# Kernel optimization log

Measured on AMD Instinct MI355X. Metric: run time of the kernel, lower is better.

Reference implementation:

```python
import math
import jax, jax.numpy as jnp
import numpy as np

DIM = 192
HEADS = 8
C_RATIO = 0.5
CR = int(DIM * C_RATIO)          # 96
HD = DIM // HEADS                # 24
CRH = CR // HEADS                # 12
SCALE = (HD * C_RATIO) ** -0.5   # qk_scale default


def conv2d(x, w, b, stride, pad, groups):
    # x: [B,C,H,W], w: [O, C//groups, kh, kw]
    y = jax.lax.conv_general_dilated(
        x, w, (stride, stride), [(pad, pad), (pad, pad)],
        dimension_numbers=('NCHW', 'OIHW', 'NCHW'),
        feature_group_count=groups)
    return y + b[None, :, None, None]


def layernorm(x, g, b, eps=1e-5):
    mu = jnp.mean(x, axis=-1, keepdims=True)
    var = jnp.mean((x - mu) ** 2, axis=-1, keepdims=True)
    return (x - mu) * jax.lax.rsqrt(var + eps) * g + b


def setup_inputs() -> dict:
    key = jax.random.key(0)
    ks = jax.random.split(key, 10)
    B, H, W = 16, 128, 128
    N = H * W
    p = lambda k, shape: jax.random.normal(k, shape, jnp.float32) * 0.02
    return {
        'x': jax.random.normal(ks[0], (B, N, DIM), jnp.float32),
        'H': H, 'W': W,
        'red_w': p(ks[1], (DIM, 1, 4, 4)), 'red_b': jnp.zeros((DIM,), jnp.float32),
        'dw_w': p(ks[2], (DIM, 1, 3, 3)), 'dw_b': jnp.zeros((DIM,), jnp.float32),
        'conv_w': p(ks[3], (DIM, DIM, 1, 1)), 'conv_b': jnp.zeros((DIM,), jnp.float32),
        'ln_g': jnp.ones((DIM,), jnp.float32), 'ln_b': jnp.zeros((DIM,), jnp.float32),
        'q_w': p(ks[4], (DIM, DIM)),
        'k_w': p(ks[5], (CR, DIM)),
        'v_w': p(ks[6], (CR, DIM)),
        'cpe_w': p(ks[7], (CR, 1, 3, 3)), 'cpe_b': jnp.zeros((CR,), jnp.float32),
        'proj_w': p(ks[8], (DIM, DIM)), 'proj_b': jnp.zeros((DIM,), jnp.float32),
    }


def reference(x, H, W, red_w, red_b, dw_w, dw_b, conv_w, conv_b,
              ln_g, ln_b, q_w, k_w, v_w, cpe_w, cpe_b, proj_w, proj_b):
    B, N, C = x.shape
    # eval-mode recursion depth (self.training == False branch)
    _time = max(int(math.log(H // 16, 4)), int(math.log(W // 16, 4)))
    _time = max(_time, 2)

    _x = jnp.swapaxes(x, 1, 2).reshape(B, C, H, W)
    for _ in range(_time):                        # recursive stride-4 depthwise reduction
        _x = conv2d(_x, red_w, red_b, 4, 0, C)
    _x = conv2d(_x, dw_w, dw_b, 1, 1, C)          # depthwise 3x3
    _x = conv2d(_x, conv_w, conv_b, 1, 0, 1)      # 1x1 mix
    _x = jnp.swapaxes(_x.reshape(B, C, -1), 1, 2)  # [B, M, C]
    _x = jax.nn.gelu(layernorm(_x, ln_g, ln_b), approximate=False)
    M = _x.shape[1]

    q = (_x @ q_w.T).reshape(B, M, HEADS, HD).transpose(0, 2, 1, 3)    # [B,h,M,hd]
    k = (_x @ k_w.T).reshape(B, M, HEADS, CRH).transpose(0, 2, 1, 3)   # [B,h,M,crh]
    v = (x @ v_w.T).reshape(B, N, HEADS, CRH).transpose(0, 2, 1, 3)    # [B,h,N,crh]

    # channel-axis attention: q^T k over reduced tokens M -> [B,h,hd,crh]
    attn = jax.nn.softmax(jnp.einsum('bhmd,bhme->bhde', q, k) * SCALE, axis=-1)

    # CPE: depthwise conv over v arranged as [B, CR, H, W], added back to v
    v_img = jnp.swapaxes(v, 1, 2).reshape(B, N, CR).transpose(0, 2, 1).reshape(B, CR, H, W)
    cpe = conv2d(v_img, cpe_w, cpe_b, 1, 1, CR).reshape(B, HEADS, CRH, N)
    v = v + jnp.swapaxes(cpe, -1, -2)             # [B,h,N,crh]

    out = jnp.einsum('bhde,bhne->bhdn', attn, v)  # attn @ v^T -> [B,h,hd,N]
    # replicate torch: .transpose(1,2).reshape(B,N,-1)
    out = jnp.swapaxes(out, 1, 2).reshape(B, N, C)
    return out @ proj_w.T + proj_b
```

## Files before the change

### kernel.cpp

```cpp
#include <hip/hip_runtime.h>
#include <hip/hip_bf16.h>
#include <math.h>

#define NB 16
#define HIMG 128
#define WIMG 128
#define NTOK 16384
#define CDIM 192
#define CRDIM 96
#define NHEAD 8
#define HDIM 24
#define CRHD 12
#define MRED 64
#define SCALE_QK 0.28867513459481287f

typedef __bf16 bf16x8 __attribute__((ext_vector_type(8)));
typedef __bf16 bf16x4 __attribute__((ext_vector_type(4)));
typedef float f32x4 __attribute__((ext_vector_type(4)));

__global__ void k_prep(const float* __restrict__ vw, const float* __restrict__ pw,
                       __bf16* __restrict__ wb) {
    int i = blockIdx.x * 256 + threadIdx.x;
    if (i < CRDIM * CDIM) wb[i] = (__bf16)vw[i];
    else if (i < CRDIM * CDIM + CDIM * CDIM) wb[i] = (__bf16)pw[i - CRDIM * CDIM];
}

__global__ __launch_bounds__(256) void k_reduce(const float* __restrict__ x,
                                                const float* __restrict__ rw,
                                                const float* __restrict__ rb,
                                                float* __restrict__ y1) {
    int idx = blockIdx.x * 256 + threadIdx.x;
    int c4 = idx % 48;
    int t  = idx / 48;
    int m  = t & 63;
    int b  = t >> 6;
    float w[16][4];
#pragma unroll
    for (int e = 0; e < 4; ++e)
#pragma unroll
        for (int i = 0; i < 16; ++i) w[i][e] = rw[(c4 * 4 + e) * 16 + i];
    int py = m >> 3, px = m & 7;
    const float4* xb = (const float4*)(x + (long)b * NTOK * CDIM) + c4;
    float acc[4] = {0.f, 0.f, 0.f, 0.f};
    for (int a = 0; a < 16; ++a) {
        const float4* xrow = xb + (long)((py * 16 + a) * WIMG + px * 16) * 48;
#pragma unroll
        for (int bb = 0; bb < 16; ++bb) {
            float4 vv = xrow[(long)bb * 48];
            int i1 = ((a >> 2) << 2) + (bb >> 2);
            int i2 = ((a & 3) << 2) + (bb & 3);
            acc[0] += w[i1][0] * w[i2][0] * vv.x;
            acc[1] += w[i1][1] * w[i2][1] * vv.y;
            acc[2] += w[i1][2] * w[i2][2] * vv.z;
            acc[3] += w[i1][3] * w[i2][3] * vv.w;
        }
    }
    float4 outv;
#pragma unroll
    for (int e = 0; e < 4; ++e) {
        float S = 0.f;
#pragma unroll
        for (int i = 0; i < 16; ++i) S += w[i][e];
        acc[e] += rb[c4 * 4 + e] * (S + 1.f);
        ((float*)&outv)[e] = acc[e];
    }
    ((float4*)(y1 + (long)(b * MRED + m) * CDIM))[c4] = outv;
}

__global__ void k_dwmix(const float* __restrict__ y1, const float* __restrict__ dww,
                        const float* __restrict__ dwb, const float* __restrict__ cw,
                        const float* __restrict__ cb, const float* __restrict__ lg,
                        const float* __restrict__ lb, float* __restrict__ xr) {
    __shared__ float sT[CDIM];
    __shared__ float sU[CDIM];
    int m = blockIdx.x, b = blockIdx.y, c = threadIdx.x;
    int py = m >> 3, px = m & 7;
    float t = dwb[c];
#pragma unroll
    for (int ki = 0; ki < 3; ++ki)
#pragma unroll
        for (int kj = 0; kj < 3; ++kj) {
            int yy = py + ki - 1, xx = px + kj - 1;
            if (yy >= 0 && yy < 8 && xx >= 0 && xx < 8)
                t += dww[c * 9 + ki * 3 + kj] * y1[(b * MRED + yy * 8 + xx) * CDIM + c];
        }
    sT[c] = t;
    __syncthreads();
    float u = cb[c];
    for (int cc = 0; cc < CDIM; ++cc) u += cw[c * CDIM + cc] * sT[cc];
    sU[c] = u;
    __syncthreads();
    float s = 0.f, s2 = 0.f;
    for (int cc = 0; cc < CDIM; ++cc) { float vv = sU[cc]; s += vv; s2 += vv * vv; }
    float mu = s * (1.f / CDIM);
    float var = fmaxf(s2 * (1.f / CDIM) - mu * mu, 0.f);
    float xh = (u - mu) * rsqrtf(var + 1e-5f);
    float g = xh * lg[c] + lb[c];
    float ge = 0.5f * g * (1.f + erff(g * 0.70710678118654752440f));
    xr[(b * MRED + m) * CDIM + c] = ge;
}

__global__ void k_qk(const float* __restrict__ xr, const float* __restrict__ qw,
                     const float* __restrict__ kw, float* __restrict__ q,
                     float* __restrict__ k) {
    __shared__ float sx[8 * 193];
    int mg = blockIdx.x;
    int b = blockIdx.y;
    int tid = threadIdx.x;
    const float* src = xr + (b * MRED + mg * 8) * CDIM;
    for (int i = tid; i < 8 * CDIM; i += 256) sx[(i / CDIM) * 193 + (i % CDIM)] = src[i];
    __syncthreads();
    for (int oi = tid; oi < 1536 + 768; oi += 256) {
        if (oi < 1536) {
            int d = oi >> 3, mi = oi & 7;
            const float* wr = qw + d * CDIM;
            const float* xs = sx + mi * 193;
            float acc = 0.f;
            for (int c = 0; c < CDIM; ++c) acc += xs[c] * wr[c];
            q[(b * MRED + mg * 8 + mi) * CDIM + d] = acc;
        } else {
            int oj = oi - 1536;
            int e = oj >> 3, mi = oj & 7;
            const float* wr = kw + e * CDIM;
            const float* xs = sx + mi * 193;
            float acc = 0.f;
            for (int c = 0; c < CDIM; ++c) acc += xs[c] * wr[c];
            k[(b * MRED + mg * 8 + mi) * CRDIM + e] = acc;
        }
    }
}

__global__ void k_attn(const float* __restrict__ q, const float* __restrict__ k,
                       float* __restrict__ attn) {
    __shared__ float sL[HDIM * CRHD];
    int h = blockIdx.x, b = blockIdx.y;
    int tid = threadIdx.x;
    for (int i = tid; i < HDIM * CRHD; i += 256) {
        int d = i / CRHD, e = i % CRHD;
        float acc = 0.f;
        for (int m = 0; m < MRED; ++m)
            acc += q[(b * MRED + m) * CDIM + h * HDIM + d] *
                   k[(b * MRED + m) * CRDIM + h * CRHD + e];
        sL[i] = acc * SCALE_QK;
    }
    __syncthreads();
    if (tid < HDIM) {
        float mx = -1e30f;
#pragma unroll
        for (int e = 0; e < CRHD; ++e) mx = fmaxf(mx, sL[tid * CRHD + e]);
        float ex[CRHD]; float sum = 0.f;
#pragma unroll
        for (int e = 0; e < CRHD; ++e) { ex[e] = expf(sL[tid * CRHD + e] - mx); sum += ex[e]; }
        float inv = 1.f / sum;
#pragma unroll
        for (int e = 0; e < CRHD; ++e)
            attn[((b * NHEAD + h) * HDIM + tid) * CRHD + e] = ex[e] * inv;
    }
}

template <int NOUT, bool ABF16, bool OUTBF16, bool BIAS>
__global__ __launch_bounds__(256) void k_gemm(const void* __restrict__ Asrc,
                                              const __bf16* __restrict__ Wb,
                                              const float* __restrict__ bias,
                                              void* __restrict__ Out) {
    static_assert(NOUT % 16 == 0, "");
    constexpr int NF = NOUT / 16;
    __shared__ __bf16 sA[64 * 200];
    __shared__ __bf16 sB[NOUT * 40];
    const int tid = threadIdx.x;
    const long rowbase = (long)blockIdx.x * 64;
    if (ABF16) {
        const __bf16* A = (const __bf16*)Asrc + rowbase * CDIM;
        for (int i = tid; i < 64 * 24; i += 256) {
            int r = i / 24, c8 = i % 24;
            bf16x8 vv = *(const bf16x8*)(A + (long)r * CDIM + c8 * 8);
            *(bf16x8*)(sA + r * 200 + c8 * 8) = vv;
        }
    } else {
        const float* A = (const float*)Asrc + rowbase * CDIM;
        for (int i = tid; i < 64 * 24; i += 256) {
            int r = i / 24, c8 = i % 24;
            const float4* src = (const float4*)(A + (long)r * CDIM + c8 * 8);
            float4 lo = src[0], hi = src[1];
            bf16x8 vv;
            vv[0] = (__bf16)lo.x; vv[1] = (__bf16)lo.y; vv[2] = (__bf16)lo.z; vv[3] = (__bf16)lo.w;
            vv[4] = (__bf16)hi.x; vv[5] = (__bf16)hi.y; vv[6] = (__bf16)hi.z; vv[7] = (__bf16)hi.w;
            *(bf16x8*)(sA + r * 200 + c8 * 8) = vv;
        }
    }
    const int lane = tid & 63, wv = tid >> 6;
    const int l16 = lane & 15, lq = lane >> 4;
    f32x4 acc[NF];
#pragma unroll
    for (int nf = 0; nf < NF; ++nf) acc[nf] = (f32x4){0.f, 0.f, 0.f, 0.f};
    const __bf16* aptr = sA + (wv * 16 + l16) * 200 + lq * 8;
    for (int kc = 0; kc < 6; ++kc) {
        __syncthreads();
        for (int i = tid; i < NOUT * 4; i += 256) {
            int r = i >> 2, c8 = i & 3;
            bf16x8 vv = *(const bf16x8*)(Wb + (long)r * CDIM + kc * 32 + c8 * 8);
            *(bf16x8*)(sB + r * 40 + c8 * 8) = vv;
        }
        __syncthreads();
        bf16x8 af = *(const bf16x8*)(aptr + kc * 32);
#pragma unroll
        for (int nf = 0; nf < NF; ++nf) {
            bf16x8 bfv = *(const bf16x8*)(sB + (nf * 16 + l16) * 40 + lq * 8);
            acc[nf] = __builtin_amdgcn_mfma_f32_16x16x32_bf16(af, bfv, acc[nf], 0, 0, 0);
        }
    }
    const long orow0 = rowbase + wv * 16 + lq * 4;
#pragma unroll
    for (int nf = 0; nf < NF; ++nf) {
        int col = nf * 16 + l16;
        float bv = BIAS ? bias[col] : 0.f;
#pragma unroll
        for (int j = 0; j < 4; ++j) {
            float val = acc[nf][j] + bv;
            long idx = (orow0 + j) * NOUT + col;
            if (OUTBF16) ((__bf16*)Out)[idx] = (__bf16)val;
            else ((float*)Out)[idx] = val;
        }
    }
}

__global__ __launch_bounds__(256) void k_cpe(const __bf16* __restrict__ v,
                                             const float* __restrict__ cw,
                                             const float* __restrict__ cb,
                                             __bf16* __restrict__ vp) {
    int idx = blockIdx.x * 256 + threadIdx.x;
    int g  = idx % 12;
    int t  = idx / 12;
    int x  = t & 127;
    int sb = t >> 7;
    int strip = sb & 15;
    int b  = sb >> 4;
    float w[9][8];
    float bias[8];
#pragma unroll
    for (int e = 0; e < 8; ++e) {
        bias[e] = cb[g * 8 + e];
#pragma unroll
        for (int tp = 0; tp < 9; ++tp) w[tp][e] = cw[(g * 8 + e) * 9 + tp];
    }
    const __bf16* vb = v + (long)b * NTOK * CRDIM + g * 8;
    __bf16* vpb = vp + (long)b * NTOK * CRDIM + g * 8;
    for (int yi = 0; yi < 8; ++yi) {
        int y = strip * 8 + yi;
        bf16x8 cv = *(const bf16x8*)(vb + (long)(y * WIMG + x) * CRDIM);
        float acc[8];
#pragma unroll
        for (int e = 0; e < 8; ++e) acc[e] = (float)cv[e] + bias[e];
#pragma unroll
        for (int ky = 0; ky < 3; ++ky) {
            int yy = y + ky - 1;
            if (yy < 0 || yy >= HIMG) continue;
#pragma unroll
            for (int kx = 0; kx < 3; ++kx) {
                int xx = x + kx - 1;
                if (xx < 0 || xx >= WIMG) continue;
                bf16x8 tv = (ky == 1 && kx == 1) ? cv
                          : *(const bf16x8*)(vb + (long)(yy * WIMG + xx) * CRDIM);
#pragma unroll
                for (int e = 0; e < 8; ++e) acc[e] += w[ky * 3 + kx][e] * (float)tv[e];
            }
        }
        bf16x8 ov;
#pragma unroll
        for (int e = 0; e < 8; ++e) ov[e] = (__bf16)acc[e];
        *(bf16x8*)(vpb + (long)(y * WIMG + x) * CRDIM) = ov;
    }
}

__global__ __launch_bounds__(256) void k_av(const __bf16* __restrict__ vp,
                                            const float* __restrict__ attn,
                                            __bf16* __restrict__ O) {
    __shared__ float sAttn[NHEAD * HDIM * CRHD];
    int chunk = blockIdx.x, b = blockIdx.y;
    int tid = threadIdx.x;
    for (int i = tid; i < NHEAD * HDIM * CRHD; i += 256)
        sAttn[i] = attn[b * NHEAD * HDIM * CRHD + i];
    __syncthreads();
    int n = chunk * 256 + tid;
    const __bf16* vrow = vp + ((long)b * NTOK + n) * CRDIM;
    __bf16* ob = O + (long)b * (HDIM * NHEAD * NTOK);
    for (int h = 0; h < NHEAD; ++h) {
        bf16x4 v0 = *(const bf16x4*)(vrow + h * CRHD);
        bf16x4 v1 = *(const bf16x4*)(vrow + h * CRHD + 4);
        bf16x4 v2 = *(const bf16x4*)(vrow + h * CRHD + 8);
        float pv[CRHD];
#pragma unroll
        for (int e = 0; e < 4; ++e) {
            pv[e] = (float)v0[e]; pv[4 + e] = (float)v1[e]; pv[8 + e] = (float)v2[e];
        }
        const float* ar = sAttn + h * HDIM * CRHD;
#pragma unroll
        for (int d = 0; d < HDIM; ++d) {
            float s = 0.f;
#pragma unroll
            for (int e = 0; e < CRHD; ++e) s += ar[d * CRHD + e] * pv[e];
            ob[(long)(d * NHEAD + h) * NTOK + n] = (__bf16)s;
        }
    }
}

extern "C" void kernel_launch(void* const* d_in, const int* in_sizes, int n_in,
                              void* d_out, int out_size, void* d_ws, size_t ws_size,
                              hipStream_t stream) {
    const float* x      = (const float*)d_in[0];
    const float* red_w  = (const float*)d_in[3];
    const float* red_b  = (const float*)d_in[4];
    const float* dw_w   = (const float*)d_in[5];
    const float* dw_b   = (const float*)d_in[6];
    const float* conv_w = (const float*)d_in[7];
    const float* conv_b = (const float*)d_in[8];
    const float* ln_g   = (const float*)d_in[9];
    const float* ln_b   = (const float*)d_in[10];
    const float* q_w    = (const float*)d_in[11];
    const float* k_w    = (const float*)d_in[12];
    const float* v_w    = (const float*)d_in[13];
    const float* cpe_w  = (const float*)d_in[14];
    const float* cpe_b  = (const float*)d_in[15];
    const float* proj_w = (const float*)d_in[16];
    const float* proj_b = (const float*)d_in[17];
    float* out = (float*)d_out;

    char* ws = (char*)d_ws;
    __bf16* wb_v = (__bf16*)ws;
    __bf16* wb_p = wb_v + CRDIM * CDIM;
    char* R = ws + 110592;
    float*  y1   = (float*)(R + 0);
    float*  xr   = (float*)(R + 786432);
    float*  qb   = (float*)(R + 1572864);
    float*  kb   = (float*)(R + 2359296);
    __bf16* v    = (__bf16*)(R + 2752512);
    __bf16* O    = (__bf16*)(R + 0);
    float*  attn = (float*)(ws + 110592 + 100663296);
    __bf16* vp   = (__bf16*)(ws + 110592 + 100663296 + 147456);

    k_prep<<<216, 256, 0, stream>>>(v_w, proj_w, wb_v);
    k_reduce<<<192, 256, 0, stream>>>(x, red_w, red_b, y1);
    k_dwmix<<<dim3(64, 16), 192, 0, stream>>>(y1, dw_w, dw_b, conv_w, conv_b, ln_g, ln_b, xr);
    k_qk<<<dim3(8, 16), 256, 0, stream>>>(xr, q_w, k_w, qb, kb);
    k_attn<<<dim3(8, 16), 256, 0, stream>>>(qb, kb, attn);
    k_gemm<CRDIM, false, true, false><<<4096, 256, 0, stream>>>(x, wb_v, nullptr, v);
    k_cpe<<<1536, 256, 0, stream>>>(v, cpe_w, cpe_b, vp);
    k_av<<<dim3(64, 16), 256, 0, stream>>>(vp, attn, O);
    k_gemm<CDIM, true, false, true><<<4096, 256, 0, stream>>>(O, wb_p, proj_b, out);
}
```

Baseline: 698.0 us.

## Fuse CPE into AV, merge QK with attention, restructure GEMM and reduction

Several changes land together. The stride-4 reduction now uses 1024 blocks, each splitting its 16 rows across 4 thread groups with a shared-memory sum, so far more parallelism is exposed. Q/K projection and channel attention become one kernel that keeps Q and K in shared memory. The CPE depthwise conv is fused into the attn@v kernel, with each thread handling two adjacent pixels, which removes the vp intermediate and one launch. The GEMM now loads the whole weight slice into LDS once, each wave computes a 2x3 MFMA tile, and the projection GEMM is split across two column halves. Costs are more LDS per block and recomputed v loads per head in the fused kernel.

Result: no change. 693.2 us (-0.7%).

```diff
diff --git a/kernel.cpp b/kernel.cpp
--- a/kernel.cpp
+++ b/kernel.cpp
@@ -16,6 +16,7 @@
 
 typedef __bf16 bf16x8 __attribute__((ext_vector_type(8)));
 typedef __bf16 bf16x4 __attribute__((ext_vector_type(4)));
+typedef __bf16 bf16x2 __attribute__((ext_vector_type(2)));
 typedef float f32x4 __attribute__((ext_vector_type(4)));
 
 __global__ void k_prep(const float* __restrict__ vw, const float* __restrict__ pw,
@@ -25,15 +26,14 @@
     else if (i < CRDIM * CDIM + CDIM * CDIM) wb[i] = (__bf16)pw[i - CRDIM * CDIM];
 }
 
-__global__ __launch_bounds__(256) void k_reduce(const float* __restrict__ x,
+__global__ __launch_bounds__(192) void k_reduce(const float* __restrict__ x,
                                                 const float* __restrict__ rw,
                                                 const float* __restrict__ rb,
                                                 float* __restrict__ y1) {
-    int idx = blockIdx.x * 256 + threadIdx.x;
-    int c4 = idx % 48;
-    int t  = idx / 48;
-    int m  = t & 63;
-    int b  = t >> 6;
+    __shared__ float4 sRed[4][48];
+    int tid = threadIdx.x;
+    int c4 = tid % 48, a4 = tid / 48;
+    int m = blockIdx.x & 63, b = blockIdx.x >> 6;
     float w[16][4];
 #pragma unroll
     for (int e = 0; e < 4; ++e)
@@ -42,7 +42,9 @@
     int py = m >> 3, px = m & 7;
     const float4* xb = (const float4*)(x + (long)b * NTOK * CDIM) + c4;
     float acc[4] = {0.f, 0.f, 0.f, 0.f};
-    for (int a = 0; a < 16; ++a) {
+#pragma unroll
+    for (int ai = 0; ai < 4; ++ai) {
+        int a = a4 * 4 + ai;
         const float4* xrow = xb + (long)((py * 16 + a) * WIMG + px * 16) * 48;
 #pragma unroll
         for (int bb = 0; bb < 16; ++bb) {
@@ -55,16 +57,22 @@
             acc[3] += w[i1][3] * w[i2][3] * vv.w;
         }
     }
-    float4 outv;
-#pragma unroll
-    for (int e = 0; e < 4; ++e) {
-        float S = 0.f;
-#pragma unroll
-        for (int i = 0; i < 16; ++i) S += w[i][e];
-        acc[e] += rb[c4 * 4 + e] * (S + 1.f);
-        ((float*)&outv)[e] = acc[e];
-    }
-    ((float4*)(y1 + (long)(b * MRED + m) * CDIM))[c4] = outv;
+    sRed[a4][c4] = make_float4(acc[0], acc[1], acc[2], acc[3]);
+    __syncthreads();
+    if (a4 == 0) {
+        float4 t0 = sRed[0][c4], t1 = sRed[1][c4], t2 = sRed[2][c4], t3 = sRed[3][c4];
+        float4 outv;
+        float r[4] = {t0.x + t1.x + t2.x + t3.x, t0.y + t1.y + t2.y + t3.y,
+                      t0.z + t1.z + t2.z + t3.z, t0.w + t1.w + t2.w + t3.w};
+#pragma unroll
+        for (int e = 0; e < 4; ++e) {
+            float S = 0.f;
+#pragma unroll
+            for (int i = 0; i < 16; ++i) S += w[i][e];
+            ((float*)&outv)[e] = r[e] + rb[c4 * 4 + e] * (S + 1.f);
+        }
+        ((float4*)(y1 + (long)(b * MRED + m) * CDIM))[c4] = outv;
+    }
 }
 
 __global__ void k_dwmix(const float* __restrict__ y1, const float* __restrict__ dww,
@@ -100,48 +108,32 @@
     xr[(b * MRED + m) * CDIM + c] = ge;
 }
 
-__global__ void k_qk(const float* __restrict__ xr, const float* __restrict__ qw,
-                     const float* __restrict__ kw, float* __restrict__ q,
-                     float* __restrict__ k) {
-    __shared__ float sx[8 * 193];
-    int mg = blockIdx.x;
-    int b = blockIdx.y;
-    int tid = threadIdx.x;
-    const float* src = xr + (b * MRED + mg * 8) * CDIM;
-    for (int i = tid; i < 8 * CDIM; i += 256) sx[(i / CDIM) * 193 + (i % CDIM)] = src[i];
-    __syncthreads();
-    for (int oi = tid; oi < 1536 + 768; oi += 256) {
-        if (oi < 1536) {
-            int d = oi >> 3, mi = oi & 7;
-            const float* wr = qw + d * CDIM;
-            const float* xs = sx + mi * 193;
-            float acc = 0.f;
-            for (int c = 0; c < CDIM; ++c) acc += xs[c] * wr[c];
-            q[(b * MRED + mg * 8 + mi) * CDIM + d] = acc;
-        } else {
-            int oj = oi - 1536;
-            int e = oj >> 3, mi = oj & 7;
-            const float* wr = kw + e * CDIM;
-            const float* xs = sx + mi * 193;
-            float acc = 0.f;
-            for (int c = 0; c < CDIM; ++c) acc += xs[c] * wr[c];
-            k[(b * MRED + mg * 8 + mi) * CRDIM + e] = acc;
-        }
-    }
-}
-
-__global__ void k_attn(const float* __restrict__ q, const float* __restrict__ k,
-                       float* __restrict__ attn) {
+__global__ __launch_bounds__(256) void k_qkattn(const float* __restrict__ xr,
+                                                const float* __restrict__ qw,
+                                                const float* __restrict__ kw,
+                                                float* __restrict__ attn) {
+    __shared__ float sX[64 * 193];
+    __shared__ float sQK[36 * 65];
     __shared__ float sL[HDIM * CRHD];
-    int h = blockIdx.x, b = blockIdx.y;
-    int tid = threadIdx.x;
-    for (int i = tid; i < HDIM * CRHD; i += 256) {
-        int d = i / CRHD, e = i % CRHD;
+    int h = blockIdx.x, b = blockIdx.y, tid = threadIdx.x;
+    const float* src = xr + (long)b * MRED * CDIM;
+    for (int i = tid; i < MRED * CDIM; i += 256) sX[(i / CDIM) * 193 + (i % CDIM)] = src[i];
+    __syncthreads();
+    for (int oi = tid; oi < 36 * 64; oi += 256) {
+        int col = oi >> 6, tok = oi & 63;
+        const float* wr = (col < 24) ? (qw + (long)(h * HDIM + col) * CDIM)
+                                     : (kw + (long)(h * CRHD + (col - 24)) * CDIM);
+        const float* xs = sX + tok * 193;
         float acc = 0.f;
-        for (int m = 0; m < MRED; ++m)
-            acc += q[(b * MRED + m) * CDIM + h * HDIM + d] *
-                   k[(b * MRED + m) * CRDIM + h * CRHD + e];
-        sL[i] = acc * SCALE_QK;
+        for (int c = 0; c < CDIM; ++c) acc += xs[c] * wr[c];
+        sQK[col * 65 + tok] = acc;
+    }
+    __syncthreads();
+    for (int oi = tid; oi < HDIM * CRHD; oi += 256) {
+        int d = oi / CRHD, e = oi % CRHD;
+        float acc = 0.f;
+        for (int t = 0; t < 64; ++t) acc += sQK[d * 65 + t] * sQK[(24 + e) * 65 + t];
+        sL[oi] = acc * SCALE_QK;
     }
     __syncthreads();
     if (tid < HDIM) {
@@ -158,148 +150,162 @@
     }
 }
 
-template <int NOUT, bool ABF16, bool OUTBF16, bool BIAS>
+template <int NOUT, int NSPLIT, bool ABF16, bool OUTBF16, bool BIAS>
 __global__ __launch_bounds__(256) void k_gemm(const void* __restrict__ Asrc,
                                               const __bf16* __restrict__ Wb,
                                               const float* __restrict__ bias,
                                               void* __restrict__ Out) {
-    static_assert(NOUT % 16 == 0, "");
-    constexpr int NF = NOUT / 16;
+    constexpr int NC = NOUT / NSPLIT;
+    constexpr int NFW = 3;
     __shared__ __bf16 sA[64 * 200];
-    __shared__ __bf16 sB[NOUT * 40];
+    __shared__ __bf16 sB[NC * 200];
     const int tid = threadIdx.x;
-    const long rowbase = (long)blockIdx.x * 64;
+    const int nh = (NSPLIT > 1) ? (int)(blockIdx.x % NSPLIT) : 0;
+    const long tile = (NSPLIT > 1) ? (blockIdx.x / NSPLIT) : blockIdx.x;
+    const long rowbase = tile * 64;
     if (ABF16) {
         const __bf16* A = (const __bf16*)Asrc + rowbase * CDIM;
         for (int i = tid; i < 64 * 24; i += 256) {
             int r = i / 24, c8 = i % 24;
-            bf16x8 vv = *(const bf16x8*)(A + (long)r * CDIM + c8 * 8);
-            *(bf16x8*)(sA + r * 200 + c8 * 8) = vv;
+            *(bf16x8*)(sA + r * 200 + c8 * 8) = *(const bf16x8*)(A + (long)r * CDIM + c8 * 8);
         }
     } else {
         const float* A = (const float*)Asrc + rowbase * CDIM;
         for (int i = tid; i < 64 * 24; i += 256) {
             int r = i / 24, c8 = i % 24;
-            const float4* src = (const float4*)(A + (long)r * CDIM + c8 * 8);
-            float4 lo = src[0], hi = src[1];
+            const float4* s4 = (const float4*)(A + (long)r * CDIM + c8 * 8);
+            float4 lo = s4[0], hi = s4[1];
             bf16x8 vv;
             vv[0] = (__bf16)lo.x; vv[1] = (__bf16)lo.y; vv[2] = (__bf16)lo.z; vv[3] = (__bf16)lo.w;
             vv[4] = (__bf16)hi.x; vv[5] = (__bf16)hi.y; vv[6] = (__bf16)hi.z; vv[7] = (__bf16)hi.w;
             *(bf16x8*)(sA + r * 200 + c8 * 8) = vv;
         }
     }
+    for (int i = tid; i < NC * 24; i += 256) {
+        int r = i / 24, c8 = i % 24;
+        *(bf16x8*)(sB + r * 200 + c8 * 8) =
+            *(const bf16x8*)(Wb + (long)(nh * NC + r) * CDIM + c8 * 8);
+    }
+    __syncthreads();
     const int lane = tid & 63, wv = tid >> 6;
     const int l16 = lane & 15, lq = lane >> 4;
-    f32x4 acc[NF];
-#pragma unroll
-    for (int nf = 0; nf < NF; ++nf) acc[nf] = (f32x4){0.f, 0.f, 0.f, 0.f};
-    const __bf16* aptr = sA + (wv * 16 + l16) * 200 + lq * 8;
-    for (int kc = 0; kc < 6; ++kc) {
-        __syncthreads();
-        for (int i = tid; i < NOUT * 4; i += 256) {
-            int r = i >> 2, c8 = i & 3;
-            bf16x8 vv = *(const bf16x8*)(Wb + (long)r * CDIM + kc * 32 + c8 * 8);
-            *(bf16x8*)(sB + r * 40 + c8 * 8) = vv;
-        }
-        __syncthreads();
-        bf16x8 af = *(const bf16x8*)(aptr + kc * 32);
-#pragma unroll
-        for (int nf = 0; nf < NF; ++nf) {
-            bf16x8 bfv = *(const bf16x8*)(sB + (nf * 16 + l16) * 40 + lq * 8);
-            acc[nf] = __builtin_amdgcn_mfma_f32_16x16x32_bf16(af, bfv, acc[nf], 0, 0, 0);
-        }
-    }
-    const long orow0 = rowbase + wv * 16 + lq * 4;
-#pragma unroll
-    for (int nf = 0; nf < NF; ++nf) {
-        int col = nf * 16 + l16;
-        float bv = BIAS ? bias[col] : 0.f;
-#pragma unroll
-        for (int j = 0; j < 4; ++j) {
-            float val = acc[nf][j] + bv;
-            long idx = (orow0 + j) * NOUT + col;
-            if (OUTBF16) ((__bf16*)Out)[idx] = (__bf16)val;
-            else ((float*)Out)[idx] = val;
-        }
-    }
-}
-
-__global__ __launch_bounds__(256) void k_cpe(const __bf16* __restrict__ v,
-                                             const float* __restrict__ cw,
-                                             const float* __restrict__ cb,
-                                             __bf16* __restrict__ vp) {
-    int idx = blockIdx.x * 256 + threadIdx.x;
-    int g  = idx % 12;
-    int t  = idx / 12;
-    int x  = t & 127;
-    int sb = t >> 7;
-    int strip = sb & 15;
-    int b  = sb >> 4;
-    float w[9][8];
-    float bias[8];
-#pragma unroll
-    for (int e = 0; e < 8; ++e) {
-        bias[e] = cb[g * 8 + e];
-#pragma unroll
-        for (int tp = 0; tp < 9; ++tp) w[tp][e] = cw[(g * 8 + e) * 9 + tp];
-    }
-    const __bf16* vb = v + (long)b * NTOK * CRDIM + g * 8;
-    __bf16* vpb = vp + (long)b * NTOK * CRDIM + g * 8;
-    for (int yi = 0; yi < 8; ++yi) {
-        int y = strip * 8 + yi;
-        bf16x8 cv = *(const bf16x8*)(vb + (long)(y * WIMG + x) * CRDIM);
-        float acc[8];
-#pragma unroll
-        for (int e = 0; e < 8; ++e) acc[e] = (float)cv[e] + bias[e];
-#pragma unroll
-        for (int ky = 0; ky < 3; ++ky) {
-            int yy = y + ky - 1;
-            if (yy < 0 || yy >= HIMG) continue;
-#pragma unroll
-            for (int kx = 0; kx < 3; ++kx) {
-                int xx = x + kx - 1;
-                if (xx < 0 || xx >= WIMG) continue;
-                bf16x8 tv = (ky == 1 && kx == 1) ? cv
-                          : *(const bf16x8*)(vb + (long)(yy * WIMG + xx) * CRDIM);
-#pragma unroll
-                for (int e = 0; e < 8; ++e) acc[e] += w[ky * 3 + kx][e] * (float)tv[e];
+    const int mi0 = (wv >> 1) * 2;
+    const int nf0 = (wv & 1) * 3;
+    f32x4 acc[2][NFW];
+#pragma unroll
+    for (int mi = 0; mi < 2; ++mi)
+#pragma unroll
+        for (int nf = 0; nf < NFW; ++nf) acc[mi][nf] = (f32x4){0.f, 0.f, 0.f, 0.f};
+    bf16x8 afr[2][6];
+#pragma unroll
+    for (int mi = 0; mi < 2; ++mi)
+#pragma unroll
+        for (int kc = 0; kc < 6; ++kc)
+            afr[mi][kc] = *(const bf16x8*)(sA + ((mi0 + mi) * 16 + l16) * 200 + kc * 32 + lq * 8);
+#pragma unroll
+    for (int kc = 0; kc < 6; ++kc)
+#pragma unroll
+        for (int nf = 0; nf < NFW; ++nf) {
+            bf16x8 bfv = *(const bf16x8*)(sB + ((nf0 + nf) * 16 + l16) * 200 + kc * 32 + lq * 8);
+#pragma unroll
+            for (int mi = 0; mi < 2; ++mi)
+                acc[mi][nf] = __builtin_amdgcn_mfma_f32_16x16x32_bf16(afr[mi][kc], bfv,
+                                                                      acc[mi][nf], 0, 0, 0);
+        }
+#pragma unroll
+    for (int mi = 0; mi < 2; ++mi) {
+        const long orow0 = rowbase + (mi0 + mi) * 16 + lq * 4;
+#pragma unroll
+        for (int nf = 0; nf < NFW; ++nf) {
+            int col = nh * NC + (nf0 + nf) * 16 + l16;
+            float bv = BIAS ? bias[col] : 0.f;
+#pragma unroll
+            for (int j = 0; j < 4; ++j) {
+                float val = acc[mi][nf][j] + bv;
+                long idx = (orow0 + j) * NOUT + col;
+                if (OUTBF16) ((__bf16*)Out)[idx] = (__bf16)val;
+                else ((float*)Out)[idx] = val;
             }
         }
-        bf16x8 ov;
-#pragma unroll
-        for (int e = 0; e < 8; ++e) ov[e] = (__bf16)acc[e];
-        *(bf16x8*)(vpb + (long)(y * WIMG + x) * CRDIM) = ov;
-    }
-}
-
-__global__ __launch_bounds__(256) void k_av(const __bf16* __restrict__ vp,
-                                            const float* __restrict__ attn,
-                                            __bf16* __restrict__ O) {
-    __shared__ float sAttn[NHEAD * HDIM * CRHD];
-    int chunk = blockIdx.x, b = blockIdx.y;
-    int tid = threadIdx.x;
+    }
+}
+
+__global__ __launch_bounds__(256) void k_avcpe(const __bf16* __restrict__ v,
+                                               const float* __restrict__ attn,
+                                               const float* __restrict__ cw,
+                                               const float* __restrict__ cb,
+                                               __bf16* __restrict__ O) {
+    __shared__ float sA2[NHEAD * HDIM * CRHD];
+    __shared__ float sW[CRDIM * 9];
+    __shared__ float sB2[CRDIM];
+    int chunk = blockIdx.x, b = blockIdx.y, tid = threadIdx.x;
     for (int i = tid; i < NHEAD * HDIM * CRHD; i += 256)
-        sAttn[i] = attn[b * NHEAD * HDIM * CRHD + i];
-    __syncthreads();
-    int n = chunk * 256 + tid;
-    const __bf16* vrow = vp + ((long)b * NTOK + n) * CRDIM;
-    __bf16* ob = O + (long)b * (HDIM * NHEAD * NTOK);
+        sA2[i] = attn[b * NHEAD * HDIM * CRHD + i];
+    for (int i = tid; i < CRDIM * 9; i += 256) sW[i] = cw[i];
+    if (tid < CRDIM) sB2[tid] = cb[tid];
+    __syncthreads();
+    int n0 = (chunk * 256 + tid) * 2;
+    int y = n0 >> 7, x = n0 & 127;
+    bool xm = (x > 0), xp = (x + 2 < WIMG);
+    const __bf16* vb = v + (long)b * NTOK * CRDIM;
+    __bf16* ob = O + (long)b * (CDIM * NTOK);
+#pragma unroll
     for (int h = 0; h < NHEAD; ++h) {
-        bf16x4 v0 = *(const bf16x4*)(vrow + h * CRHD);
-        bf16x4 v1 = *(const bf16x4*)(vrow + h * CRHD + 4);
-        bf16x4 v2 = *(const bf16x4*)(vrow + h * CRHD + 8);
-        float pv[CRHD];
-#pragma unroll
-        for (int e = 0; e < 4; ++e) {
-            pv[e] = (float)v0[e]; pv[4 + e] = (float)v1[e]; pv[8 + e] = (float)v2[e];
-        }
-        const float* ar = sAttn + h * HDIM * CRHD;
+        float vp0[CRHD], vp1[CRHD];
+#pragma unroll
+        for (int e = 0; e < CRHD; ++e) { vp0[e] = sB2[h * CRHD + e]; vp1[e] = vp0[e]; }
+#pragma unroll
+        for (int rr = 0; rr < 3; ++rr) {
+            int ry = y + rr - 1;
+            if (ry < 0 || ry >= HIMG) continue;
+            const __bf16* rowp = vb + ((long)ry * WIMG) * CRDIM + h * CRHD;
+#pragma unroll
+            for (int cc = 0; cc < 4; ++cc) {
+                int cx = x + cc - 1;
+                bool valid = (cc > 0 || xm) && (cc < 3 || xp);
+                float tv[CRHD];
+                if (valid) {
+                    const __bf16* p = rowp + (long)cx * CRDIM;
+                    bf16x4 t0 = *(const bf16x4*)(p);
+                    bf16x4 t1 = *(const bf16x4*)(p + 4);
+                    bf16x4 t2 = *(const bf16x4*)(p + 8);
+#pragma unroll
+                    for (int e = 0; e < 4; ++e) {
+                        tv[e] = (float)t0[e]; tv[4 + e] = (float)t1[e]; tv[8 + e] = (float)t2[e];
+                    }
+                } else {
+#pragma unroll
+                    for (int e = 0; e < CRHD; ++e) tv[e] = 0.f;
+                }
+                if (cc < 3) {
+#pragma unroll
+                    for (int e = 0; e < CRHD; ++e)
+                        vp0[e] += sW[(h * CRHD + e) * 9 + rr * 3 + cc] * tv[e];
+                    if (rr == 1 && cc == 1)
+#pragma unroll
+                        for (int e = 0; e < CRHD; ++e) vp0[e] += tv[e];
+                }
+                if (cc > 0) {
+#pragma unroll
+                    for (int e = 0; e < CRHD; ++e)
+                        vp1[e] += sW[(h * CRHD + e) * 9 + rr * 3 + cc - 1] * tv[e];
+                    if (rr == 1 && cc == 2)
+#pragma unroll
+                        for (int e = 0; e < CRHD; ++e) vp1[e] += tv[e];
+                }
+            }
+        }
+        const float* ar = sA2 + h * HDIM * CRHD;
 #pragma unroll
         for (int d = 0; d < HDIM; ++d) {
-            float s = 0.f;
-#pragma unroll
-            for (int e = 0; e < CRHD; ++e) s += ar[d * CRHD + e] * pv[e];
-            ob[(long)(d * NHEAD + h) * NTOK + n] = (__bf16)s;
+            float s0 = 0.f, s1 = 0.f;
+#pragma unroll
+            for (int e = 0; e < CRHD; ++e) {
+                float a = ar[d * CRHD + e];
+                s0 += a * vp0[e]; s1 += a * vp1[e];
+            }
+            bf16x2 o2; o2[0] = (__bf16)s0; o2[1] = (__bf16)s1;
+            *(bf16x2*)(ob + (long)(d * NHEAD + h) * NTOK + n0) = o2;
         }
     }
 }
@@ -327,24 +333,18 @@
 
     char* ws = (char*)d_ws;
     __bf16* wb_v = (__bf16*)ws;
-    __bf16* wb_p = wb_v + CRDIM * CDIM;
-    char* R = ws + 110592;
-    float*  y1   = (float*)(R + 0);
-    float*  xr   = (float*)(R + 786432);
-    float*  qb   = (float*)(R + 1572864);
-    float*  kb   = (float*)(R + 2359296);
-    __bf16* v    = (__bf16*)(R + 2752512);
-    __bf16* O    = (__bf16*)(R + 0);
-    float*  attn = (float*)(ws + 110592 + 100663296);
-    __bf16* vp   = (__bf16*)(ws + 110592 + 100663296 + 147456);
+    __bf16* wb_p = (__bf16*)(ws + 36864);
+    float*  y1   = (float*)(ws + 110592);
+    float*  xr   = (float*)(ws + 897024);
+    float*  attn = (float*)(ws + 1683456);
+    __bf16* v    = (__bf16*)(ws + 1830912);
+    __bf16* O    = (__bf16*)(ws + 52162560);
 
     k_prep<<<216, 256, 0, stream>>>(v_w, proj_w, wb_v);
-    k_reduce<<<192, 256, 0, stream>>>(x, red_w, red_b, y1);
+    k_reduce<<<1024, 192, 0, stream>>>(x, red_w, red_b, y1);
     k_dwmix<<<dim3(64, 16), 192, 0, stream>>>(y1, dw_w, dw_b, conv_w, conv_b, ln_g, ln_b, xr);
-    k_qk<<<dim3(8, 16), 256, 0, stream>>>(xr, q_w, k_w, qb, kb);
-    k_attn<<<dim3(8, 16), 256, 0, stream>>>(qb, kb, attn);
-    k_gemm<CRDIM, false, true, false><<<4096, 256, 0, stream>>>(x, wb_v, nullptr, v);
-    k_cpe<<<1536, 256, 0, stream>>>(v, cpe_w, cpe_b, vp);
-    k_av<<<dim3(64, 16), 256, 0, stream>>>(vp, attn, O);
-    k_gemm<CDIM, true, false, true><<<4096, 256, 0, stream>>>(O, wb_p, proj_b, out);
-}
+    k_qkattn<<<dim3(8, 16), 256, 0, stream>>>(xr, q_w, k_w, attn);
+    k_gemm<CRDIM, 1, false, true, false><<<4096, 256, 0, stream>>>(x, wb_v, nullptr, v);
+    k_avcpe<<<dim3(32, 16), 256, 0, stream>>>(v, attn, cpe_w, cpe_b, O);
+    k_gemm<CDIM, 2, true, false, true><<<8192, 256, 0, stream>>>(O, wb_p, proj_b, out);
+}
```
